# Kernel tuning notes

Measured on AMD Instinct MI355X. Metric: run time of the kernel, lower is better.

## Reference

```python
import jax, jax.numpy as jnp
import numpy as np

B, T, HID = 2, 2048, 3840
H, KV, D = 16, 8, 256
EPS = 1e-6
WINDOW = 1024
THETA_LOCAL = 10000.0
THETA_GLOBAL = 1000000.0


def _rope_tables(theta, t, d):
    inv_freq = 1.0 / (theta ** (jnp.arange(0, d, 2, dtype=jnp.float32) / d))  # (d/2,)
    ang = jnp.arange(t, dtype=jnp.float32)[:, None] * inv_freq[None, :]        # (T, d/2)
    return jnp.cos(ang), jnp.sin(ang)


def setup_inputs() -> dict:
    key = jax.random.key(0)
    ks = jax.random.split(key, 8)
    x = jax.random.normal(ks[0], (B, T, HID), dtype=jnp.float32)
    wq = jax.random.normal(ks[1], (H * D, HID), dtype=jnp.float32) * 0.02
    wk = jax.random.normal(ks[2], (KV * D, HID), dtype=jnp.float32) * 0.02
    wv = jax.random.normal(ks[3], (KV * D, HID), dtype=jnp.float32) * 0.02
    wo = jax.random.normal(ks[4], (HID, H * D), dtype=jnp.float32) * 0.02
    q_norm_w = 1.0 + jax.random.normal(ks[5], (D,), dtype=jnp.float32) * 0.02
    k_norm_w = 1.0 + jax.random.normal(ks[6], (D,), dtype=jnp.float32) * 0.02
    cos_g, sin_g = _rope_tables(THETA_GLOBAL, T, D)
    cos_l, sin_l = _rope_tables(THETA_LOCAL, T, D)
    # causal + sliding-window(1024) additive float mask, shape (1,1,T,T)
    i = jnp.arange(T)[:, None]
    j = jnp.arange(T)[None, :]
    allowed = (j <= i) & (i - j < WINDOW)
    attention_mask = jnp.where(allowed, 0.0, -1e9).astype(jnp.float32)[None, None]
    return {"x": x, "cos_global": cos_g, "sin_global": sin_g, "cos_local": cos_l,
            "sin_local": sin_l, "attention_mask": attention_mask,
            "wq": wq, "wk": wk, "wv": wv, "wo": wo,
            "q_norm_w": q_norm_w, "k_norm_w": k_norm_w}


def _rms_norm(x, w):
    # add=False variant: x * rsqrt(mean(x^2)+eps) * w, computed in fp32
    norm = jax.lax.rsqrt(jnp.mean(jnp.square(x), axis=-1, keepdims=True) + EPS)
    return x * norm * w


def _apply_rope(x, cos, sin):
    # x: (B, H, T, D); cos/sin: (T, D/2)
    t = x.shape[2]
    c = cos[:t][None, None]
    s = sin[:t][None, None]
    x1, x2 = x[..., : x.shape[-1] // 2], x[..., x.shape[-1] // 2 :]
    return jnp.concatenate([x1 * c - x2 * s, x2 * c + x1 * s], axis=-1)


def reference(x, cos_global, sin_global, cos_local, sin_local, attention_mask,
              wq, wk, wv, wo, q_norm_w, k_norm_w):
    b, t, _ = x.shape
    q = (x @ wq.T).reshape(b, t, H, D).transpose(0, 2, 1, 3)   # (B,H,T,D)
    k = (x @ wk.T).reshape(b, t, KV, D).transpose(0, 2, 1, 3)  # (B,KV,T,D)
    v = (x @ wv.T).reshape(b, t, KV, D).transpose(0, 2, 1, 3)
    q = _rms_norm(q, q_norm_w)
    k = _rms_norm(k, k_norm_w)
    # layer_idx=0 -> sliding-window layer -> local rope
    q = _apply_rope(q, cos_local, sin_local)
    k = _apply_rope(k, cos_local, sin_local)
    rep = H // KV
    k = jnp.repeat(k, rep, axis=1)  # repeat_interleave over head dim
    v = jnp.repeat(v, rep, axis=1)
    scale = 1.0 / jnp.sqrt(jnp.float32(D))
    scores = jnp.einsum("bhqd,bhkd->bhqk", q, k) * scale + attention_mask
    attn = jax.nn.softmax(scores, axis=-1)
    out = jnp.einsum("bhqk,bhkd->bhqd", attn, v)
    out = out.transpose(0, 2, 1, 3).reshape(b, t, H * D)
    return out @ wo.T
```

## Files before the change

kernel.cpp:

```cpp
#include <hip/hip_runtime.h>
#include <hip/hip_bf16.h>

typedef __hip_bfloat16 BF;
typedef __attribute__((ext_vector_type(8))) short short8;
typedef __attribute__((ext_vector_type(4))) float f32x4;

#define DEV __device__ __forceinline__

DEV void gll16(const BF* g, BF* l) {
  __builtin_amdgcn_global_load_lds(
      (const __attribute__((address_space(1))) void*)g,
      (__attribute__((address_space(3))) void*)l, 16, 0, 0);
}

DEV void stage2(const BF* src, size_t rstp, BF* dst) {
  gll16(src, dst);
  gll16(src + rstp, dst + 4096);
}

DEV unsigned short bfbits(float f) {
  BF b = __float2bfloat16(f);
  return *reinterpret_cast<unsigned short*>(&b);
}

__global__ void f32_to_bf16_k(const float* __restrict__ in, BF* __restrict__ out, int n4) {
  int i = blockIdx.x * blockDim.x + threadIdx.x;
  if (i >= n4) return;
  const float4 v = ((const float4*)in)[i];
  ((ushort4*)out)[i] = make_ushort4(bfbits(v.x), bfbits(v.y), bfbits(v.z), bfbits(v.w));
}

#define PHASE(MH, KK, STAGE, TAIL)                                                   \
  {                                                                                  \
    short8 af[4], bfr[4];                                                            \
    const BF* Ap = Ax + (KK)*8192;                                                   \
    const BF* Bp = Bx + (KK)*8192;                                                   \
    _Pragma("unroll") for (int m = 0; m < 4; ++m)                                    \
        af[m] = *(const short8*)&Ap[(wm*128 + (MH)*64 + m*16 + l15) * 32 + rd8];     \
    _Pragma("unroll") for (int n = 0; n < 4; ++n)                                    \
        bfr[n] = *(const short8*)&Bp[(wn*64 + n*16 + l15) * 32 + rd8];               \
    STAGE                                                                            \
    __builtin_amdgcn_s_barrier();                                                    \
    asm volatile("s_waitcnt lgkmcnt(0)" ::: "memory");                               \
    __builtin_amdgcn_sched_barrier(0);                                               \
    __builtin_amdgcn_s_setprio(1);                                                   \
    _Pragma("unroll") for (int m = 0; m < 4; ++m)                                    \
      _Pragma("unroll") for (int n = 0; n < 4; ++n)                                  \
        acc[(MH)*4 + m][n] =                                                         \
            __builtin_amdgcn_mfma_f32_16x16x32_bf16(af[m], bfr[n], acc[(MH)*4+m][n], 0, 0, 0); \
    __builtin_amdgcn_s_setprio(0);                                                   \
    TAIL                                                                             \
    __builtin_amdgcn_s_barrier();                                                    \
  }

template <typename CT>
__global__ __launch_bounds__(512, 2) void gemm256_bt(const BF* __restrict__ A,
                                                     const BF* __restrict__ Bm,
                                                     CT* __restrict__ C,
                                                     const int M, const int N, const int K) {
  extern __shared__ __align__(16) BF lds[];
  BF* ldsA = lds;
  BF* ldsB = lds + 32768;
  const int ntl = N >> 8;
  const int cpx = gridDim.x >> 3;
  const int swzb = (blockIdx.x & 7) * cpx + (blockIdx.x >> 3);
  const int mt = swzb / ntl, nt = swzb % ntl;
  const int m0 = mt << 8, n0 = nt << 8;
  const int tid = threadIdx.x, lane = tid & 63, w = tid >> 6;
  const int l15 = lane & 15, g = lane >> 4;
  const int wm = w >> 2, wn = w & 3;
  const int rd8 = (g ^ ((l15 >> 1) & 3)) << 3;
  const int trow = tid >> 2;
  const int scol = ((lane & 3) ^ ((lane >> 3) & 3)) << 3;
  const BF* aS = A + (size_t)(m0 + trow) * K + scol;
  const BF* bS = Bm + (size_t)(n0 + trow) * K + scol;
  const size_t rstp = (size_t)128 * K;
  BF* dA = ldsA + w * 512;
  BF* dB = ldsB + w * 512;
  const int NT = K >> 6;

  f32x4 acc[8][4];
#pragma unroll
  for (int m = 0; m < 8; ++m)
#pragma unroll
    for (int n = 0; n < 4; ++n) acc[m][n] = (f32x4){0.f, 0.f, 0.f, 0.f};

  stage2(aS, rstp, dA);
  stage2(bS, rstp, dB);
  stage2(aS + 32, rstp, dA + 8192);
  stage2(bS + 32, rstp, dB + 8192);
  stage2(aS + 64, rstp, dA + 16384);
  stage2(bS + 64, rstp, dB + 16384);
  asm volatile("s_waitcnt vmcnt(8)" ::: "memory");
  __builtin_amdgcn_sched_barrier(0);
  __builtin_amdgcn_s_barrier();

  for (int t = 0; t < NT; ++t) {
    const int bX = (t & 1) << 14;
    const int bY = bX ^ 16384;
    const BF* Ax = ldsA + bX;
    const BF* Bx = ldsB + bX;
    const int kc1 = (t + 1) << 6, kc2 = (t + 2) << 6;
    const bool s1 = (t + 1 < NT), s2 = (t + 2 < NT);
    PHASE(0, 0, if (s1) stage2(aS + kc1 + 32, rstp, dA + bY + 8192);, )
    PHASE(1, 0, if (s1) stage2(bS + kc1 + 32, rstp, dB + bY + 8192);,
          { asm volatile("s_waitcnt vmcnt(8)" ::: "memory");
            __builtin_amdgcn_sched_barrier(0); } )
    PHASE(0, 1, if (s2) stage2(aS + kc2, rstp, dA + bX);, )
    PHASE(1, 1, if (s2) stage2(bS + kc2, rstp, dB + bX);,
          if (s2) { asm volatile("s_waitcnt vmcnt(8)" ::: "memory");
                    __builtin_amdgcn_sched_barrier(0); }
          else    { asm volatile("s_waitcnt vmcnt(0)" ::: "memory");
                    __builtin_amdgcn_sched_barrier(0); } )
  }

#pragma unroll
  for (int mi = 0; mi < 8; ++mi) {
    const int gr = m0 + wm * 128 + mi * 16 + g * 4;
#pragma unroll
    for (int n = 0; n < 4; ++n) {
      const int gc = n0 + wn * 64 + n * 16 + l15;
#pragma unroll
      for (int r = 0; r < 4; ++r) {
        const float v = acc[mi][n][r];
        if constexpr (sizeof(CT) == 2)
          C[(size_t)(gr + r) * N + gc] = __float2bfloat16(v);
        else
          C[(size_t)(gr + r) * N + gc] = v;
      }
    }
  }
}

__global__ __launch_bounds__(256) void rmsrope(const BF* __restrict__ C1,
                                               BF* __restrict__ Qo, BF* __restrict__ Ko,
                                               const float* __restrict__ cosl,
                                               const float* __restrict__ sinl,
                                               const float* __restrict__ qw,
                                               const float* __restrict__ kw) {
  const int gwid = (blockIdx.x * 256 + threadIdx.x) >> 6;
  const int lane = threadIdx.x & 63;
  const int slot = gwid % 24;
  const int bt = gwid / 24;
  const int b = bt >> 11, t = bt & 2047;
  const BF* src;
  BF* dst;
  const float* wgt;
  if (slot < 16) {
    src = C1 + (size_t)bt * 8192 + slot * 256;
    dst = Qo + ((size_t)(b * 16 + slot) * 2048 + t) * 256;
    wgt = qw;
  } else {
    const int kv = slot - 16;
    src = C1 + (size_t)bt * 8192 + 4096 + kv * 256;
    dst = Ko + ((size_t)(b * 8 + kv) * 2048 + t) * 256;
    wgt = kw;
  }
  const int d2 = lane * 2;
  const ushort2 lo = *(const ushort2*)((const unsigned short*)src + d2);
  const ushort2 hi = *(const ushort2*)((const unsigned short*)src + 128 + d2);
  float x0 = __bfloat162float(*(const BF*)&lo.x);
  float x1 = __bfloat162float(*(const BF*)&lo.y);
  float x2 = __bfloat162float(*(const BF*)&hi.x);
  float x3 = __bfloat162float(*(const BF*)&hi.y);
  float ss = x0 * x0 + x1 * x1 + x2 * x2 + x3 * x3;
#pragma unroll
  for (int mm = 32; mm >= 1; mm >>= 1) ss += __shfl_xor(ss, mm);
  const float nrm = rsqrtf(ss * (1.f / 256.f) + 1e-6f);
  const float2 wlo = *(const float2*)(wgt + d2);
  const float2 whi = *(const float2*)(wgt + 128 + d2);
  x0 *= nrm * wlo.x;
  x1 *= nrm * wlo.y;
  x2 *= nrm * whi.x;
  x3 *= nrm * whi.y;
  const float2 c = *(const float2*)(cosl + t * 128 + d2);
  const float2 s = *(const float2*)(sinl + t * 128 + d2);
  ushort2 olo, ohi;
  olo.x = bfbits(x0 * c.x - x2 * s.x);
  olo.y = bfbits(x1 * c.y - x3 * s.y);
  ohi.x = bfbits(x2 * c.x + x0 * s.x);
  ohi.y = bfbits(x3 * c.y + x1 * s.y);
  *(ushort2*)((unsigned short*)dst + d2) = olo;
  *(ushort2*)((unsigned short*)dst + 128 + d2) = ohi;
}

__global__ void vtrans(const BF* __restrict__ C1, BF* __restrict__ Vt) {
  __shared__ BF tile[32][33];
  const int bz = blockIdx.z;
  const int tt = blockIdx.x;
  const int dt = blockIdx.y;
  const int x = threadIdx.x, y0 = threadIdx.y;
  const int b = bz >> 3, kv = bz & 7;
#pragma unroll
  for (int yy = y0; yy < 32; yy += 8) {
    const int t = tt * 32 + yy, d = dt * 32 + x;
    tile[yy][x] = C1[((size_t)(b * 2048 + t)) * 8192 + 6144 + kv * 256 + d];
  }
  __syncthreads();
#pragma unroll
  for (int yy = y0; yy < 32; yy += 8) {
    const int d = dt * 32 + yy, t = tt * 32 + x;
    Vt[((size_t)bz * 256 + d) * 2048 + t] = tile[x][yy];
  }
}

__global__ __launch_bounds__(256, 2) void attn_fwd(const BF* __restrict__ Q,
                                                   const BF* __restrict__ K,
                                                   const BF* __restrict__ Vt,
                                                   BF* __restrict__ O) {
  __shared__ __align__(16) BF Ks[64 * 256];
  __shared__ __align__(16) BF Vs[256 * 64];
  __shared__ __align__(16) BF Ps[4][1024];
  const int tid = threadIdx.x;
  const int lane = tid & 63;
  const int w = tid >> 6;
  const int l15 = lane & 15;
  const int g = lane >> 4;
  const int qt = blockIdx.x;
  const int bh = blockIdx.y;
  const int b = bh >> 4, h = bh & 15;
  const int kvh = h >> 1;
  const int q0 = qt << 6;
  const BF* Qb = Q + ((size_t)bh * 2048 + q0) * 256;
  const BF* Kb = K + (size_t)(b * 8 + kvh) * 2048 * 256;
  const BF* Vb = Vt + (size_t)(b * 8 + kvh) * 256 * 2048;

  short8 qf[8];
  {
    const BF* qr = Qb + (w * 16 + l15) * 256 + g * 8;
#pragma unroll
    for (int kk = 0; kk < 8; ++kk) qf[kk] = *(const short8*)(qr + kk * 32);
  }
  f32x4 oacc[16];
#pragma unroll
  for (int i = 0; i < 16; ++i) oacc[i] = (f32x4){0.f, 0.f, 0.f, 0.f};
  float m_r[4] = {-1e30f, -1e30f, -1e30f, -1e30f};
  float l_r[4] = {0.f, 0.f, 0.f, 0.f};

  const int kt_lo = (q0 > 1023) ? ((q0 - 1023) >> 6) : 0;
  for (int kt = kt_lo; kt <= qt; ++kt) {
    const int tk = kt << 6;
#pragma unroll
    for (int i = 0; i < 8; ++i) {
      const int li = w * 8 + i;
      {
        const int row = li * 2 + (lane >> 5);
        const int ch = lane & 31;
        gll16(Kb + (size_t)(tk + row) * 256 + ((ch ^ (row & 7)) << 3), Ks + li * 512);
      }
      {
        const int row = li * 8 + (lane >> 3);
        const int ch = lane & 7;
        gll16(Vb + (size_t)row * 2048 + tk + ((ch ^ (row & 7)) << 3), Vs + li * 512);
      }
    }
    __syncthreads();

    f32x4 sa[4];
#pragma unroll
    for (int i2 = 0; i2 < 4; ++i2) sa[i2] = (f32x4){0.f, 0.f, 0.f, 0.f};
#pragma unroll
    for (int kk = 0; kk < 8; ++kk) {
      const int d = kk * 32 + g * 8;
#pragma unroll
      for (int blk = 0; blk < 4; ++blk) {
        const int row = blk * 16 + l15;
        const short8 kf = *(const short8*)&Ks[row * 256 + (d ^ ((row & 7) << 3))];
        sa[blk] = __builtin_amdgcn_mfma_f32_16x16x32_bf16(qf[kk], kf, sa[blk], 0, 0, 0);
      }
    }

    float al4[4];
#pragma unroll
    for (int r = 0; r < 4; ++r) {
      const int qi = q0 + w * 16 + g * 4 + r;
      float pv[4];
      float tmax = -1e30f;
#pragma unroll
      for (int blk = 0; blk < 4; ++blk) {
        const int ki = tk + blk * 16 + l15;
        float sv = sa[blk][r] * 0.0625f;
        const bool ok = (ki <= qi) && (qi - ki < 1024);
        sv = ok ? sv : -1e30f;
        pv[blk] = sv;
        tmax = fmaxf(tmax, sv);
      }
#pragma unroll
      for (int mm = 1; mm < 16; mm <<= 1) tmax = fmaxf(tmax, __shfl_xor(tmax, mm));
      const float mn = fmaxf(m_r[r], tmax);
      const float alpha = __expf(m_r[r] - mn);
      float tsum = 0.f;
#pragma unroll
      for (int blk = 0; blk < 4; ++blk) {
        const float p = __expf(pv[blk] - mn);
        pv[blk] = p;
        tsum += p;
      }
#pragma unroll
      for (int mm = 1; mm < 16; mm <<= 1) tsum += __shfl_xor(tsum, mm);
      l_r[r] = l_r[r] * alpha + tsum;
      m_r[r] = mn;
      al4[r] = alpha;
      const int prow = g * 4 + r;
#pragma unroll
      for (int blk = 0; blk < 4; ++blk) {
        const int col = blk * 16 + l15;
        Ps[w][prow * 64 + (col ^ ((prow & 7) << 3))] = __float2bfloat16(pv[blk]);
      }
    }
#pragma unroll
    for (int db = 0; db < 16; ++db)
#pragma unroll
      for (int r = 0; r < 4; ++r) oacc[db][r] *= al4[r];

#pragma unroll
    for (int kk2 = 0; kk2 < 2; ++kk2) {
      const int k8 = kk2 * 32 + g * 8;
      const short8 pf = *(const short8*)&Ps[w][l15 * 64 + (k8 ^ ((l15 & 7) << 3))];
#pragma unroll
      for (int db = 0; db < 16; ++db) {
        const int vrow = db * 16 + l15;
        const short8 vf = *(const short8*)&Vs[vrow * 64 + (k8 ^ ((vrow & 7) << 3))];
        oacc[db] = __builtin_amdgcn_mfma_f32_16x16x32_bf16(pf, vf, oacc[db], 0, 0, 0);
      }
    }
    __syncthreads();
  }

#pragma unroll
  for (int r = 0; r < 4; ++r) l_r[r] = 1.f / l_r[r];
  const size_t orow0 = (size_t)(b * 2048 + q0 + w * 16 + g * 4);
#pragma unroll
  for (int r = 0; r < 4; ++r) {
    BF* op = O + (orow0 + r) * 4096 + h * 256 + l15;
#pragma unroll
    for (int db = 0; db < 16; ++db) op[db * 16] = __float2bfloat16(oacc[db][r] * l_r[r]);
  }
}

extern "C" void kernel_launch(void* const* d_in, const int* in_sizes, int n_in,
                              void* d_out, int out_size, void* d_ws, size_t ws_size,
                              hipStream_t stream) {
  (void)in_sizes; (void)n_in; (void)out_size;
  const float* x    = (const float*)d_in[0];
  const float* cosl = (const float*)d_in[3];
  const float* sinl = (const float*)d_in[4];
  const float* wq   = (const float*)d_in[6];
  const float* wk   = (const float*)d_in[7];
  const float* wv   = (const float*)d_in[8];
  const float* wo   = (const float*)d_in[9];
  const float* qw   = (const float*)d_in[10];
  const float* kw   = (const float*)d_in[11];
  float* out = (float*)d_out;
  char* ws = (char*)d_ws;
  if (ws_size < 192937984ull) return;

  BF* Wqkv = (BF*)(ws + 0);
  BF* Wo   = (BF*)(ws + 62914560);
  BF* Xbf  = (BF*)(ws + 94371840);
  BF* C1   = (BF*)(ws + 125829120);
  BF* Qb   = (BF*)(ws + 0);
  BF* Kb   = (BF*)(ws + 33554432);
  BF* Vt   = (BF*)(ws + 94371840);
  BF* AO   = (BF*)(ws + 125829120);

  hipFuncSetAttribute(reinterpret_cast<const void*>(gemm256_bt<BF>),
                      hipFuncAttributeMaxDynamicSharedMemorySize, 131072);
  hipFuncSetAttribute(reinterpret_cast<const void*>(gemm256_bt<float>),
                      hipFuncAttributeMaxDynamicSharedMemorySize, 131072);

  auto cvt = [&](const float* src, BF* dst, int n) {
    const int n4 = n >> 2;
    f32_to_bf16_k<<<(n4 + 255) / 256, 256, 0, stream>>>(src, dst, n4);
  };
  cvt(x,  Xbf, 4096 * 3840);
  cvt(wq, Wqkv, 4096 * 3840);
  cvt(wk, Wqkv + 4096 * 3840, 2048 * 3840);
  cvt(wv, Wqkv + 6144 * 3840, 2048 * 3840);
  cvt(wo, Wo, 3840 * 4096);

  gemm256_bt<BF><<<512, 512, 131072, stream>>>(Xbf, Wqkv, C1, 4096, 8192, 3840);
  rmsrope<<<24576, 256, 0, stream>>>(C1, Qb, Kb, cosl, sinl, qw, kw);
  vtrans<<<dim3(64, 8, 16), dim3(32, 8), 0, stream>>>(C1, Vt);
  attn_fwd<<<dim3(32, 32), 256, 0, stream>>>(Qb, Kb, Vt, AO);
  gemm256_bt<float><<<240, 512, 131072, stream>>>(AO, Wo, out, 4096, 3840, 4096);
}
```

Measured before the change: 601.0 us.

## Pad out-projection operand strides and reuse B fragments across M halves

The GEMM now takes separate leading dimensions for A and B. The attention output and the converted Wo are stored with a padded row stride of 4160 instead of 4096, which avoids power-of-two stride conflicts in the cache and channels for the final GEMM. The GEMM phase loads B fragments from LDS once per K half and keeps them in registers for both M halves, which cuts LDS reads but holds more registers live. The workspace layout is also reshuffled, and the Wo conversion is moved after the QKV GEMM.

```diff
diff --git a/kernel.cpp b/kernel.cpp
--- a/kernel.cpp
+++ b/kernel.cpp
@@ -11,11 +11,6 @@
   __builtin_amdgcn_global_load_lds(
       (const __attribute__((address_space(1))) void*)g,
       (__attribute__((address_space(3))) void*)l, 16, 0, 0);
-}
-
-DEV void stage2(const BF* src, size_t rstp, BF* dst) {
-  gll16(src, dst);
-  gll16(src + rstp, dst + 4096);
 }
 
 DEV unsigned short bfbits(float f) {
@@ -30,15 +25,26 @@
   ((ushort4*)out)[i] = make_ushort4(bfbits(v.x), bfbits(v.y), bfbits(v.z), bfbits(v.w));
 }
 
-#define PHASE(MH, KK, STAGE, TAIL)                                                   \
+__global__ void f32_to_bf16_pad_k(const float* __restrict__ in, BF* __restrict__ out, int n4) {
+  int i = blockIdx.x * blockDim.x + threadIdx.x;
+  if (i >= n4) return;
+  const float4 v = ((const float4*)in)[i];
+  const int r = i >> 10;
+  const int c = i & 1023;
+  ((ushort4*)out)[r * 1040 + c] = make_ushort4(bfbits(v.x), bfbits(v.y), bfbits(v.z), bfbits(v.w));
+}
+
+#define PHASE(MH, KK, READB, STAGE, TAIL)                                            \
   {                                                                                  \
-    short8 af[4], bfr[4];                                                            \
+    short8 af[4];                                                                    \
     const BF* Ap = Ax + (KK)*8192;                                                   \
-    const BF* Bp = Bx + (KK)*8192;                                                   \
     _Pragma("unroll") for (int m = 0; m < 4; ++m)                                    \
         af[m] = *(const short8*)&Ap[(wm*128 + (MH)*64 + m*16 + l15) * 32 + rd8];     \
-    _Pragma("unroll") for (int n = 0; n < 4; ++n)                                    \
-        bfr[n] = *(const short8*)&Bp[(wn*64 + n*16 + l15) * 32 + rd8];               \
+    if (READB) {                                                                     \
+      const BF* Bp = Bx + (KK)*8192;                                                 \
+      _Pragma("unroll") for (int n = 0; n < 4; ++n)                                  \
+          breg[n] = *(const short8*)&Bp[(wn*64 + n*16 + l15) * 32 + rd8];            \
+    }                                                                                \
     STAGE                                                                            \
     __builtin_amdgcn_s_barrier();                                                    \
     asm volatile("s_waitcnt lgkmcnt(0)" ::: "memory");                               \
@@ -47,7 +53,7 @@
     _Pragma("unroll") for (int m = 0; m < 4; ++m)                                    \
       _Pragma("unroll") for (int n = 0; n < 4; ++n)                                  \
         acc[(MH)*4 + m][n] =                                                         \
-            __builtin_amdgcn_mfma_f32_16x16x32_bf16(af[m], bfr[n], acc[(MH)*4+m][n], 0, 0, 0); \
+            __builtin_amdgcn_mfma_f32_16x16x32_bf16(af[m], breg[n], acc[(MH)*4+m][n], 0, 0, 0); \
     __builtin_amdgcn_s_setprio(0);                                                   \
     TAIL                                                                             \
     __builtin_amdgcn_s_barrier();                                                    \
@@ -57,7 +63,8 @@
 __global__ __launch_bounds__(512, 2) void gemm256_bt(const BF* __restrict__ A,
                                                      const BF* __restrict__ Bm,
                                                      CT* __restrict__ C,
-                                                     const int M, const int N, const int K) {
+                                                     const int M, const int N, const int K,
+                                                     const int lda, const int ldb) {
   extern __shared__ __align__(16) BF lds[];
   BF* ldsA = lds;
   BF* ldsB = lds + 32768;
@@ -72,9 +79,10 @@
   const int rd8 = (g ^ ((l15 >> 1) & 3)) << 3;
   const int trow = tid >> 2;
   const int scol = ((lane & 3) ^ ((lane >> 3) & 3)) << 3;
-  const BF* aS = A + (size_t)(m0 + trow) * K + scol;
-  const BF* bS = Bm + (size_t)(n0 + trow) * K + scol;
-  const size_t rstp = (size_t)128 * K;
+  const BF* aS = A + (size_t)(m0 + trow) * lda + scol;
+  const BF* bS = Bm + (size_t)(n0 + trow) * ldb + scol;
+  const size_t rstpA = (size_t)128 * lda;
+  const size_t rstpB = (size_t)128 * ldb;
   BF* dA = ldsA + w * 512;
   BF* dB = ldsB + w * 512;
   const int NT = K >> 6;
@@ -84,13 +92,16 @@
   for (int m = 0; m < 8; ++m)
 #pragma unroll
     for (int n = 0; n < 4; ++n) acc[m][n] = (f32x4){0.f, 0.f, 0.f, 0.f};
-
-  stage2(aS, rstp, dA);
-  stage2(bS, rstp, dB);
-  stage2(aS + 32, rstp, dA + 8192);
-  stage2(bS + 32, rstp, dB + 8192);
-  stage2(aS + 64, rstp, dA + 16384);
-  stage2(bS + 64, rstp, dB + 16384);
+  short8 breg[4];
+
+#define STG2(SRC, RST, DST) { gll16((SRC), (DST)); gll16((SRC) + (RST), (DST) + 4096); }
+
+  STG2(aS, rstpA, dA);
+  STG2(bS, rstpB, dB);
+  STG2(aS + 32, rstpA, dA + 8192);
+  STG2(bS + 32, rstpB, dB + 8192);
+  STG2(aS + 64, rstpA, dA + 16384);
+  STG2(bS + 64, rstpB, dB + 16384);
   asm volatile("s_waitcnt vmcnt(8)" ::: "memory");
   __builtin_amdgcn_sched_barrier(0);
   __builtin_amdgcn_s_barrier();
@@ -102,12 +113,12 @@
     const BF* Bx = ldsB + bX;
     const int kc1 = (t + 1) << 6, kc2 = (t + 2) << 6;
     const bool s1 = (t + 1 < NT), s2 = (t + 2 < NT);
-    PHASE(0, 0, if (s1) stage2(aS + kc1 + 32, rstp, dA + bY + 8192);, )
-    PHASE(1, 0, if (s1) stage2(bS + kc1 + 32, rstp, dB + bY + 8192);,
+    PHASE(0, 0, 1, if (s1) STG2(aS + kc1 + 32, rstpA, dA + bY + 8192);, )
+    PHASE(1, 0, 0, if (s1) STG2(bS + kc1 + 32, rstpB, dB + bY + 8192);,
           { asm volatile("s_waitcnt vmcnt(8)" ::: "memory");
             __builtin_amdgcn_sched_barrier(0); } )
-    PHASE(0, 1, if (s2) stage2(aS + kc2, rstp, dA + bX);, )
-    PHASE(1, 1, if (s2) stage2(bS + kc2, rstp, dB + bX);,
+    PHASE(0, 1, 1, if (s2) STG2(aS + kc2, rstpA, dA + bX);, )
+    PHASE(1, 1, 0, if (s2) STG2(bS + kc2, rstpB, dB + bX);,
           if (s2) { asm volatile("s_waitcnt vmcnt(8)" ::: "memory");
                     __builtin_amdgcn_sched_barrier(0); }
           else    { asm volatile("s_waitcnt vmcnt(0)" ::: "memory");
@@ -332,7 +343,7 @@
   const size_t orow0 = (size_t)(b * 2048 + q0 + w * 16 + g * 4);
 #pragma unroll
   for (int r = 0; r < 4; ++r) {
-    BF* op = O + (orow0 + r) * 4096 + h * 256 + l15;
+    BF* op = O + (orow0 + r) * 4160 + h * 256 + l15;
 #pragma unroll
     for (int db = 0; db < 16; ++db) op[db * 16] = __float2bfloat16(oacc[db][r] * l_r[r]);
   }
@@ -353,16 +364,16 @@
   const float* kw   = (const float*)d_in[11];
   float* out = (float*)d_out;
   char* ws = (char*)d_ws;
-  if (ws_size < 192937984ull) return;
+  if (ws_size < 161480704ull) return;
 
   BF* Wqkv = (BF*)(ws + 0);
-  BF* Wo   = (BF*)(ws + 62914560);
-  BF* Xbf  = (BF*)(ws + 94371840);
-  BF* C1   = (BF*)(ws + 125829120);
+  BF* Xbf  = (BF*)(ws + 62914560);
+  BF* C1   = (BF*)(ws + 94371840);
   BF* Qb   = (BF*)(ws + 0);
   BF* Kb   = (BF*)(ws + 33554432);
-  BF* Vt   = (BF*)(ws + 94371840);
-  BF* AO   = (BF*)(ws + 125829120);
+  BF* Vt   = (BF*)(ws + 62914560);
+  BF* AO   = (BF*)(ws + 94371840);
+  BF* Wo   = (BF*)(ws + 128450560);
 
   hipFuncSetAttribute(reinterpret_cast<const void*>(gemm256_bt<BF>),
                       hipFuncAttributeMaxDynamicSharedMemorySize, 131072);
@@ -377,11 +388,14 @@
   cvt(wq, Wqkv, 4096 * 3840);
   cvt(wk, Wqkv + 4096 * 3840, 2048 * 3840);
   cvt(wv, Wqkv + 6144 * 3840, 2048 * 3840);
-  cvt(wo, Wo, 3840 * 4096);
-
-  gemm256_bt<BF><<<512, 512, 131072, stream>>>(Xbf, Wqkv, C1, 4096, 8192, 3840);
+
+  gemm256_bt<BF><<<512, 512, 131072, stream>>>(Xbf, Wqkv, C1, 4096, 8192, 3840, 3840, 3840);
   rmsrope<<<24576, 256, 0, stream>>>(C1, Qb, Kb, cosl, sinl, qw, kw);
   vtrans<<<dim3(64, 8, 16), dim3(32, 8), 0, stream>>>(C1, Vt);
+  {
+    const int n4 = (3840 * 4096) >> 2;
+    f32_to_bf16_pad_k<<<(n4 + 255) / 256, 256, 0, stream>>>(wo, Wo, n4);
+  }
   attn_fwd<<<dim3(32, 32), 256, 0, stream>>>(Qb, Kb, Vt, AO);
-  gemm256_bt<float><<<240, 512, 131072, stream>>>(AO, Wo, out, 4096, 3840, 4096);
-}
+  gemm256_bt<float><<<240, 512, 131072, stream>>>(AO, Wo, out, 4096, 3840, 4096, 4160, 4160);
+}
```

Measured after the change: 585.7 us. 1.03x faster.
